# Optimization experiments

Hardware: AMD Instinct MI355X
Metric: run time of the kernel (lower is better)

## Reference

```python
import jax, jax.numpy as jnp
import numpy as np

N, E, F, C, K, H = 100000, 1600000, 64, 32, 8, 36


def setup_inputs() -> dict:
    key = jax.random.key(0)
    ks = jax.random.split(key, 24)
    s = 0.1
    inp = {
        "x": jax.random.normal(ks[0], (N, F), jnp.float32),
        "edge_index": jax.random.randint(ks[1], (2, E), 0, N, dtype=jnp.int32),
        # ChebConv conv1_1: K x [F, H] weights + bias
        "W1_1": jax.random.normal(ks[2], (K, F, H), jnp.float32) * s,
        "b1_1": jnp.zeros((H,), jnp.float32),
        "g1_1": jnp.ones((H,), jnp.float32),
        "be1_1": jnp.zeros((H,), jnp.float32),
        # ChebConv conv1_2: K x [H, H]
        "W1_2": jax.random.normal(ks[3], (K, H, H), jnp.float32) * s,
        "b1_2": jnp.zeros((H,), jnp.float32),
        "g1_2": jnp.ones((H,), jnp.float32),
        "be1_2": jnp.zeros((H,), jnp.float32),
        # GINConv MLP: Linear(F,H) -> ReLU -> Linear(H,H)
        "gin_w1": jax.random.normal(ks[4], (F, H), jnp.float32) * s,
        "gin_b1": jnp.zeros((H,), jnp.float32),
        "gin_w2": jax.random.normal(ks[5], (H, H), jnp.float32) * s,
        "gin_b2": jnp.zeros((H,), jnp.float32),
        "g2": jnp.ones((H,), jnp.float32),
        "be2": jnp.zeros((H,), jnp.float32),
        # conv4: ChebConv K=1 on concat(3H) -> C  (pure linear, no propagation)
        "W4": jax.random.normal(ks[6], (1, 3 * H, C), jnp.float32) * s,
        "b4": jnp.zeros((C,), jnp.float32),
    }
    return inp


def _spmm(w, src, dst, x, n):
    # out[i] = sum_{e: dst_e=i} w_e * x[src_e]
    return jax.ops.segment_sum(w[:, None] * x[src], dst, num_segments=n)


def _cheb(x, src, dst, w, Wk, b):
    # PyG ChebConv with sym norm, lambda_max=2: L_hat = -D^-1/2 A D^-1/2 (loop weight 0)
    n = x.shape[0]
    Kk = Wk.shape[0]
    Tx0 = x
    out = Tx0 @ Wk[0]
    if Kk > 1:
        Tx1 = _spmm(w, src, dst, Tx0, n)
        out = out + Tx1 @ Wk[1]
        for k in range(2, Kk):
            Tx2 = 2.0 * _spmm(w, src, dst, Tx1, n) - Tx0
            out = out + Tx2 @ Wk[k]
            Tx0, Tx1 = Tx1, Tx2
    return out + b


def _bn(x, g, b, eps=1e-5):
    m = jnp.mean(x, axis=0)
    v = jnp.mean(jnp.square(x - m), axis=0)  # biased var, training-mode BN
    return g * (x - m) * jax.lax.rsqrt(v + eps) + b


def reference(x, edge_index, W1_1, b1_1, g1_1, be1_1, W1_2, b1_2, g1_2, be1_2,
              gin_w1, gin_b1, gin_w2, gin_b2, g2, be2, W4, b4):
    src, dst = edge_index[0], edge_index[1]
    n = x.shape[0]
    deg = jax.ops.segment_sum(jnp.ones((src.shape[0],), x.dtype), src, num_segments=n)
    dis = jnp.where(deg > 0, jax.lax.rsqrt(jnp.maximum(deg, 1.0)), 0.0)
    w = -dis[src] * dis[dst]  # scaled Laplacian edge weights

    x1_1 = jax.nn.relu(_bn(_cheb(x, src, dst, w, W1_1, b1_1), g1_1, be1_1))
    x1_2 = jax.nn.relu(_bn(_cheb(x1_1, src, dst, w, W1_2, b1_2), g1_2, be1_2))

    # GINConv (eps=0): nn(x + sum_{j in N(i)} x_j)
    agg = jax.ops.segment_sum(x[src], dst, num_segments=n)
    h = x + agg
    gin = jax.nn.relu(h @ gin_w1 + gin_b1) @ gin_w2 + gin_b2
    x2 = _bn(jax.nn.relu(gin), g2, be2)

    x4 = jnp.concatenate((x1_1, x1_2, x2), axis=1)
    return x4 @ W4[0] + b4
```

## Files before the change

### kernel.cpp

```cpp
#include <hip/hip_runtime.h>

constexpr int N_NODES = 100000;
constexpr int N_EDGES = 1600000;
constexpr int NBK  = 391;
constexpr int NBLK = 640;
constexpr int CHUNK = 2500;
constexpr int LCNT = NBK * NBLK;
constexpr int SCAN_BLKS = (LCNT + 255) / 256;


__device__ __forceinline__ unsigned bf16pack(float a, float b) {
    unsigned ua = __float_as_uint(a), ub = __float_as_uint(b);
    ua += 0x7fffu + ((ua >> 16) & 1u);
    ub += 0x7fffu + ((ub >> 16) & 1u);
    return (ua >> 16) | (ub & 0xffff0000u);
}
__device__ __forceinline__ float bflo(unsigned p) { return __uint_as_float(p << 16); }
__device__ __forceinline__ float bfhi(unsigned p) { return __uint_as_float(p & 0xffff0000u); }

__device__ __forceinline__ int esrc(unsigned v) { return (int)(v & 0x1FFFFu); }
__device__ __forceinline__ float ew(unsigned v) {
    return __uint_as_float(0x80000000u | ((v >> 17) << 16));
}


__global__ __launch_bounds__(256) void part_count_kernel(
    const int* __restrict__ ei, int* __restrict__ cntD, int* __restrict__ cntS) {
    __shared__ int hd[NBK], hs[NBK];
    int tid = threadIdx.x;
    for (int i = tid; i < NBK; i += 256) { hd[i] = 0; hs[i] = 0; }
    __syncthreads();
    int e0 = blockIdx.x * CHUNK;
    for (int e = e0 + tid; e < e0 + CHUNK; e += 256) {
        int s = ei[e], d = ei[N_EDGES + e];
        atomicAdd(&hs[s >> 8], 1);
        atomicAdd(&hd[d >> 8], 1);
    }
    __syncthreads();
    for (int i = tid; i < NBK; i += 256) {
        cntD[i * NBLK + blockIdx.x] = hd[i];
        cntS[i * NBLK + blockIdx.x] = hs[i];
    }
}

__global__ __launch_bounds__(256) void scanA_kernel(const int* __restrict__ in,
                                                    int* __restrict__ out,
                                                    int* __restrict__ bsum, int L) {
    __shared__ int sm[256];
    int i = blockIdx.x * 256 + threadIdx.x;
    int v = (i < L) ? in[i] : 0;
    sm[threadIdx.x] = v;
    __syncthreads();
    for (int off = 1; off < 256; off <<= 1) {
        int t = (threadIdx.x >= off) ? sm[threadIdx.x - off] : 0;
        __syncthreads();
        sm[threadIdx.x] += t;
        __syncthreads();
    }
    if (i < L) out[i] = sm[threadIdx.x] - v;
    if (threadIdx.x == 255) bsum[blockIdx.x] = sm[255];
}

__global__ __launch_bounds__(1024) void scanB_kernel(int* __restrict__ bsum, int nb) {
    __shared__ int sm[1024];
    int t = threadIdx.x;
    int v = (t < nb) ? bsum[t] : 0;
    sm[t] = v;
    __syncthreads();
    for (int off = 1; off < 1024; off <<= 1) {
        int u = (t >= off) ? sm[t - off] : 0;
        __syncthreads();
        sm[t] += u;
        __syncthreads();
    }
    if (t < nb) bsum[t] = sm[t] - v;
}

__global__ __launch_bounds__(256) void scanC_kernel(int* __restrict__ out,
                                                    const int* __restrict__ bsum, int L) {
    int i = blockIdx.x * 256 + threadIdx.x;
    if (i < L) out[i] += bsum[blockIdx.x];
}

__global__ __launch_bounds__(256) void part_scatter_kernel(
    const int* __restrict__ ei, const int* __restrict__ scanD,
    const int* __restrict__ scanS, int2* __restrict__ edgepart,
    int* __restrict__ srcpart) {
    __shared__ int curD[NBK], curS[NBK];
    int tid = threadIdx.x;
    for (int i = tid; i < NBK; i += 256) {
        curD[i] = scanD[i * NBLK + blockIdx.x];
        curS[i] = scanS[i * NBLK + blockIdx.x];
    }
    __syncthreads();
    int e0 = blockIdx.x * CHUNK;
    for (int e = e0 + tid; e < e0 + CHUNK; e += 256) {
        int s = ei[e], d = ei[N_EDGES + e];
        int pd = atomicAdd(&curD[d >> 8], 1);
        edgepart[pd] = make_int2(s, d);
        int ps = atomicAdd(&curS[s >> 8], 1);
        srcpart[ps] = s;
    }
}

__global__ __launch_bounds__(256) void deg_kernel(const int* __restrict__ srcpart,
                                                  const int* __restrict__ scanS,
                                                  float* __restrict__ dis) {
    __shared__ int cnt[256];
    int b = blockIdx.x, tid = threadIdx.x;
    cnt[tid] = 0;
    __syncthreads();
    int beg = scanS[b * NBLK];
    int end = (b + 1 < NBK) ? scanS[(b + 1) * NBLK] : N_EDGES;
    for (int j = beg + tid; j < end; j += 256)
        atomicAdd(&cnt[srcpart[j] & 255], 1);
    __syncthreads();
    int node = b * 256 + tid;
    if (node < N_NODES) dis[node] = cnt[tid] > 0 ? rsqrtf((float)cnt[tid]) : 0.f;
}

__global__ __launch_bounds__(256) void csr_kernel(const int2* __restrict__ edgepart,
                                                  const int* __restrict__ scanD,
                                                  const float* __restrict__ dis,
                                                  int* __restrict__ rp,
                                                  unsigned* __restrict__ csrc) {
    __shared__ int cnt[256];
    __shared__ int lofs[256];
    __shared__ float disl[256];
    int b = blockIdx.x, tid = threadIdx.x;
    int beg = scanD[b * NBLK];
    int end = (b + 1 < NBK) ? scanD[(b + 1) * NBLK] : N_EDGES;
    int node = b * 256 + tid;
    cnt[tid] = 0;
    disl[tid] = (node < N_NODES) ? dis[node] : 0.f;
    __syncthreads();
    for (int j = beg + tid; j < end; j += 256)
        atomicAdd(&cnt[edgepart[j].y & 255], 1);
    __syncthreads();
    int v = cnt[tid];
    lofs[tid] = v;
    __syncthreads();
    for (int off = 1; off < 256; off <<= 1) {
        int t = (tid >= off) ? lofs[tid - off] : 0;
        __syncthreads();
        lofs[tid] += t;
        __syncthreads();
    }
    int myexc = lofs[tid] - v;
    if (node < N_NODES) rp[node] = beg + myexc;
    if (b == NBK - 1 && tid == 0) rp[N_NODES] = N_EDGES;
    __syncthreads();
    lofs[tid] = myexc;
    cnt[tid] = 0;
    __syncthreads();
    for (int j = beg + tid; j < end; j += 256) {
        int2 e = edgepart[j];
        int dl = e.y & 255;
        int pos = beg + lofs[dl] + atomicAdd(&cnt[dl], 1);
        unsigned u = __float_as_uint(-(dis[e.x] * disl[dl]));
        u += 0x7fffu + ((u >> 16) & 1u);
        unsigned wb = (u >> 16) & 0x7FFFu;
        csrc[pos] = (unsigned)e.x | (wb << 17);
    }
}

__global__ void pack_x_kernel(const float* __restrict__ x, uint2* __restrict__ xbf) {
    int i = blockIdx.x * blockDim.x + threadIdx.x;
    if (i >= N_NODES * 16) return;
    float4 v = ((const float4*)x)[i];
    xbf[i] = make_uint2(bf16pack(v.x, v.y), bf16pack(v.z, v.w));
}


template <int FI, int SCALE, bool HAS_B2, bool BN_A, bool FUSE_STATS>
__global__ __launch_bounds__(256) void cheb_step_kernel(
    const int* __restrict__ rp, const unsigned* __restrict__ csrc,
    const uint2* __restrict__ INb, const uint2* __restrict__ B2b,
    const uint2* __restrict__ Ab, const float* __restrict__ W,
    const float* __restrict__ ss, unsigned long long* __restrict__ OUT,
    float* __restrict__ partials) {
    constexpr int RU2 = FI / 4;
    __shared__ float Wl[FI * 36];
    __shared__ float Atile[28][FI + 1];
    __shared__ float ls[72];
    int tid = threadIdx.x;
    for (int i = tid; i < FI * 36; i += 252) Wl[i] = W[i];
    int r0 = blockIdx.x * 28;
    const long long* ab8 = (const long long*)Ab;
    for (int i = tid; i < 28 * RU2; i += 252) {
        int r = i / RU2, u = i % RU2;
        int row = r0 + r;
        long long av = (row < N_NODES) ? ab8[(size_t)row * RU2 + u] : 0LL;
        unsigned lo = (unsigned)av, hi = (unsigned)(av >> 32);
        float f0 = bflo(lo), f1 = bfhi(lo), f2 = bflo(hi), f3 = bfhi(hi);
        if (BN_A) {
            int f = u * 4;
            f0 = fmaxf(fmaf(ss[f + 0], f0, ss[36 + f + 0]), 0.f);
            f1 = fmaxf(fmaf(ss[f + 1], f1, ss[36 + f + 1]), 0.f);
            f2 = fmaxf(fmaf(ss[f + 2], f2, ss[36 + f + 2]), 0.f);
            f3 = fmaxf(fmaf(ss[f + 3], f3, ss[36 + f + 3]), 0.f);
        }
        Atile[r][u * 4 + 0] = f0; Atile[r][u * 4 + 1] = f1;
        Atile[r][u * 4 + 2] = f2; Atile[r][u * 4 + 3] = f3;
    }
    if (FUSE_STATS && tid < 72) ls[tid] = 0.f;
    __syncthreads();
    int r = tid / 9, c = tid % 9;
    int row = r0 + r;
    bool valid = row < N_NODES;
    float ax = 0, ay = 0, az = 0, aw = 0;
    float bx = 0, by = 0, bz = 0, bw = 0;
    float cx = 0, cy = 0, cz = 0, cw = 0;
    float dx = 0, dy = 0, dz = 0, dw = 0;
    if (SCALE != 0 && valid) {
        int beg = rp[row], end = rp[row + 1];
        int j = beg;
        for (; j + 7 < end; j += 8) {
            unsigned v0 = csrc[j],     v1 = csrc[j + 1], v2 = csrc[j + 2], v3 = csrc[j + 3];
            unsigned v4 = csrc[j + 4], v5 = csrc[j + 5], v6 = csrc[j + 6], v7 = csrc[j + 7];
            uint2 u0 = INb[(size_t)esrc(v0) * 9 + c];
            uint2 u1 = INb[(size_t)esrc(v1) * 9 + c];
            uint2 u2 = INb[(size_t)esrc(v2) * 9 + c];
            uint2 u3 = INb[(size_t)esrc(v3) * 9 + c];
            uint2 u4 = INb[(size_t)esrc(v4) * 9 + c];
            uint2 u5 = INb[(size_t)esrc(v5) * 9 + c];
            uint2 u6 = INb[(size_t)esrc(v6) * 9 + c];
            uint2 u7 = INb[(size_t)esrc(v7) * 9 + c];
            float w0 = ew(v0), w1 = ew(v1), w2 = ew(v2), w3 = ew(v3);
            float w4 = ew(v4), w5 = ew(v5), w6 = ew(v6), w7 = ew(v7);
            ax = fmaf(w0, bflo(u0.x), ax); ay = fmaf(w0, bfhi(u0.x), ay);
            az = fmaf(w0, bflo(u0.y), az); aw = fmaf(w0, bfhi(u0.y), aw);
            bx = fmaf(w1, bflo(u1.x), bx); by = fmaf(w1, bfhi(u1.x), by);
            bz = fmaf(w1, bflo(u1.y), bz); bw = fmaf(w1, bfhi(u1.y), bw);
            cx = fmaf(w2, bflo(u2.x), cx); cy = fmaf(w2, bfhi(u2.x), cy);
            cz = fmaf(w2, bflo(u2.y), cz); cw = fmaf(w2, bfhi(u2.y), cw);
            dx = fmaf(w3, bflo(u3.x), dx); dy = fmaf(w3, bfhi(u3.x), dy);
            dz = fmaf(w3, bflo(u3.y), dz); dw = fmaf(w3, bfhi(u3.y), dw);
            ax = fmaf(w4, bflo(u4.x), ax); ay = fmaf(w4, bfhi(u4.x), ay);
            az = fmaf(w4, bflo(u4.y), az); aw = fmaf(w4, bfhi(u4.y), aw);
            bx = fmaf(w5, bflo(u5.x), bx); by = fmaf(w5, bfhi(u5.x), by);
            bz = fmaf(w5, bflo(u5.y), bz); bw = fmaf(w5, bfhi(u5.y), bw);
            cx = fmaf(w6, bflo(u6.x), cx); cy = fmaf(w6, bfhi(u6.x), cy);
            cz = fmaf(w6, bflo(u6.y), cz); cw = fmaf(w6, bfhi(u6.y), cw);
            dx = fmaf(w7, bflo(u7.x), dx); dy = fmaf(w7, bfhi(u7.x), dy);
            dz = fmaf(w7, bflo(u7.y), dz); dw = fmaf(w7, bfhi(u7.y), dw);
        }
        for (; j < end; ++j) {
            unsigned v = csrc[j];
            uint2 u = INb[(size_t)esrc(v) * 9 + c];
            float w = ew(v);
            ax = fmaf(w, bflo(u.x), ax); ay = fmaf(w, bfhi(u.x), ay);
            az = fmaf(w, bflo(u.y), az); aw = fmaf(w, bfhi(u.y), aw);
        }
        ax += bx + cx + dx; ay += by + cy + dy;
        az += bz + cz + dz; aw += bw + cw + dw;
    }
    float px = 0, py = 0, pz = 0, pw = 0;
    const float4* Wl4 = (const float4*)Wl;
#pragma unroll 4
    for (int f = 0; f < FI; ++f) {
        float a = Atile[r][f];
        float4 wv = Wl4[f * 9 + c];
        px = fmaf(a, wv.x, px); py = fmaf(a, wv.y, py);
        pz = fmaf(a, wv.z, pz); pw = fmaf(a, wv.w, pw);
    }
    const float S = (float)SCALE;
    float4 o;
    o.x = fmaf(S, ax, px); o.y = fmaf(S, ay, py);
    o.z = fmaf(S, az, pz); o.w = fmaf(S, aw, pw);
    if (valid) {
        if (HAS_B2) {
            uint2 u = B2b[(size_t)row * 9 + c];
            o.x -= bflo(u.x); o.y -= bfhi(u.x);
            o.z -= bflo(u.y); o.w -= bfhi(u.y);
        }
        unsigned long long pv = (unsigned long long)bf16pack(o.x, o.y)
                              | ((unsigned long long)bf16pack(o.z, o.w) << 32);
        OUT[(size_t)row * 9 + c] = pv;
        if (FUSE_STATS) {
            atomicAdd(&ls[c * 4 + 0], o.x); atomicAdd(&ls[36 + c * 4 + 0], o.x * o.x);
            atomicAdd(&ls[c * 4 + 1], o.y); atomicAdd(&ls[36 + c * 4 + 1], o.y * o.y);
            atomicAdd(&ls[c * 4 + 2], o.z); atomicAdd(&ls[36 + c * 4 + 2], o.z * o.z);
            atomicAdd(&ls[c * 4 + 3], o.w); atomicAdd(&ls[36 + c * 4 + 3], o.w * o.w);
        }
    }
    if (FUSE_STATS) {
        __syncthreads();
        if (tid < 72) partials[blockIdx.x * 72 + tid] = ls[tid];
    }
}


__global__ __launch_bounds__(256) void gin_gather_kernel(
    const int* __restrict__ rp, const unsigned* __restrict__ csrc,
    const uint2* __restrict__ Yb, const float* __restrict__ b1,
    const float* __restrict__ w2, const float* __restrict__ b2,
    unsigned long long* __restrict__ OUT, float* __restrict__ partials) {
    __shared__ float W2l[36 * 36];
    __shared__ float B1l[36], B2l[36];
    __shared__ float M1t[28][37];
    __shared__ float ls[72];
    int tid = threadIdx.x;
    for (int i = tid; i < 36 * 36; i += 252) W2l[i] = w2[i];
    if (tid < 36) { B1l[tid] = b1[tid]; B2l[tid] = b2[tid]; }
    if (tid < 72) ls[tid] = 0.f;
    __syncthreads();
    int r = tid / 9, c = tid % 9;
    int row = blockIdx.x * 28 + r;
    bool valid = row < N_NODES;
    float ax = 0, ay = 0, az = 0, aw = 0;
    float bx = 0, by = 0, bz = 0, bw = 0;
    float cx = 0, cy = 0, cz = 0, cw = 0;
    float dx = 0, dy = 0, dz = 0, dw = 0;
    if (valid) {
        uint2 us = Yb[(size_t)row * 9 + c];
        ax = bflo(us.x); ay = bfhi(us.x); az = bflo(us.y); aw = bfhi(us.y);
        int beg = rp[row], end = rp[row + 1];
        int j = beg;
        for (; j + 7 < end; j += 8) {
            int s0 = esrc(csrc[j]),     s1 = esrc(csrc[j + 1]);
            int s2 = esrc(csrc[j + 2]), s3 = esrc(csrc[j + 3]);
            int s4 = esrc(csrc[j + 4]), s5 = esrc(csrc[j + 5]);
            int s6 = esrc(csrc[j + 6]), s7 = esrc(csrc[j + 7]);
            uint2 u0 = Yb[(size_t)s0 * 9 + c];
            uint2 u1 = Yb[(size_t)s1 * 9 + c];
            uint2 u2 = Yb[(size_t)s2 * 9 + c];
            uint2 u3 = Yb[(size_t)s3 * 9 + c];
            uint2 u4 = Yb[(size_t)s4 * 9 + c];
            uint2 u5 = Yb[(size_t)s5 * 9 + c];
            uint2 u6 = Yb[(size_t)s6 * 9 + c];
            uint2 u7 = Yb[(size_t)s7 * 9 + c];
            ax += bflo(u0.x) + bflo(u4.x); ay += bfhi(u0.x) + bfhi(u4.x);
            az += bflo(u0.y) + bflo(u4.y); aw += bfhi(u0.y) + bfhi(u4.y);
            bx += bflo(u1.x) + bflo(u5.x); by += bfhi(u1.x) + bfhi(u5.x);
            bz += bflo(u1.y) + bflo(u5.y); bw += bfhi(u1.y) + bfhi(u5.y);
            cx += bflo(u2.x) + bflo(u6.x); cy += bfhi(u2.x) + bfhi(u6.x);
            cz += bflo(u2.y) + bflo(u6.y); cw += bfhi(u2.y) + bfhi(u6.y);
            dx += bflo(u3.x) + bflo(u7.x); dy += bfhi(u3.x) + bfhi(u7.x);
            dz += bflo(u3.y) + bflo(u7.y); dw += bfhi(u3.y) + bfhi(u7.y);
        }
        for (; j < end; ++j) {
            uint2 u = Yb[(size_t)esrc(csrc[j]) * 9 + c];
            ax += bflo(u.x); ay += bfhi(u.x);
            az += bflo(u.y); aw += bfhi(u.y);
        }
        ax += bx + cx + dx; ay += by + cy + dy;
        az += bz + cz + dz; aw += bw + cw + dw;
    }
    float m0 = fmaxf(ax + B1l[c * 4 + 0], 0.f);
    float m1 = fmaxf(ay + B1l[c * 4 + 1], 0.f);
    float m2 = fmaxf(az + B1l[c * 4 + 2], 0.f);
    float m3 = fmaxf(aw + B1l[c * 4 + 3], 0.f);
    M1t[r][c * 4 + 0] = m0; M1t[r][c * 4 + 1] = m1;
    M1t[r][c * 4 + 2] = m2; M1t[r][c * 4 + 3] = m3;
    __syncthreads();
    float o0 = B2l[c * 4 + 0], o1 = B2l[c * 4 + 1];
    float o2 = B2l[c * 4 + 2], o3 = B2l[c * 4 + 3];
    const float4* W2l4 = (const float4*)W2l;
#pragma unroll 4
    for (int f = 0; f < 36; ++f) {
        float a = M1t[r][f];
        float4 wv = W2l4[f * 9 + c];
        o0 = fmaf(a, wv.x, o0); o1 = fmaf(a, wv.y, o1);
        o2 = fmaf(a, wv.z, o2); o3 = fmaf(a, wv.w, o3);
    }
    o0 = fmaxf(o0, 0.f); o1 = fmaxf(o1, 0.f);
    o2 = fmaxf(o2, 0.f); o3 = fmaxf(o3, 0.f);
    if (valid) {
        unsigned long long pv = (unsigned long long)bf16pack(o0, o1)
                              | ((unsigned long long)bf16pack(o2, o3) << 32);
        OUT[(size_t)row * 9 + c] = pv;
        atomicAdd(&ls[c * 4 + 0], o0); atomicAdd(&ls[36 + c * 4 + 0], o0 * o0);
        atomicAdd(&ls[c * 4 + 1], o1); atomicAdd(&ls[36 + c * 4 + 1], o1 * o1);
        atomicAdd(&ls[c * 4 + 2], o2); atomicAdd(&ls[36 + c * 4 + 2], o2 * o2);
        atomicAdd(&ls[c * 4 + 3], o3); atomicAdd(&ls[36 + c * 4 + 3], o3 * o3);
    }
    __syncthreads();
    if (tid < 72) partials[blockIdx.x * 72 + tid] = ls[tid];
}


__global__ __launch_bounds__(256) void finalize_kernel(
    const float* __restrict__ partials, int nb, const float* __restrict__ g,
    const float* __restrict__ be, float* __restrict__ ss) {
    __shared__ float rs[256], rq[256];
    int c = blockIdx.x;
    int t = threadIdx.x;
    float s = 0.f, q = 0.f;
    for (int i = t; i < nb; i += 256) {
        s += partials[i * 72 + c];
        q += partials[i * 72 + c + 36];
    }
    rs[t] = s; rq[t] = q;
    __syncthreads();
    for (int off = 128; off > 0; off >>= 1) {
        if (t < off) { rs[t] += rs[t + off]; rq[t] += rq[t + off]; }
        __syncthreads();
    }
    if (t == 0) {
        float m = rs[0] / (float)N_NODES;
        float v = rq[0] / (float)N_NODES - m * m;
        float sc = g[c] * rsqrtf(v + 1e-5f);
        ss[c] = sc;
        ss[36 + c] = be[c] - m * sc;
    }
}


__global__ __launch_bounds__(256) void fused3_kernel(
    const uint2* __restrict__ X1b, const float* __restrict__ ssA,
    const uint2* __restrict__ X2b, const float* __restrict__ ssB,
    const uint2* __restrict__ X3b, const float* __restrict__ ssC,
    const float* __restrict__ W, const float* __restrict__ b,
    float* __restrict__ out) {
    __shared__ float Wl[108 * 32];
    __shared__ float Al[32][109];
    int tid = threadIdx.x;
    for (int i = tid; i < 108 * 32; i += 256) Wl[i] = W[i];
    int r0 = blockIdx.x * 32;
    for (int i = tid; i < 32 * 108; i += 256) {
        int r = i / 108, f = i % 108;
        int row = r0 + r;
        float v = 0.f;
        if (row < N_NODES) {
            int t = f / 36, ff = f % 36;
            const unsigned short* base =
                (const unsigned short*)(t == 0 ? X1b : (t == 1 ? X2b : X3b));
            float xv = __uint_as_float((unsigned)base[(size_t)row * 36 + ff] << 16);
            if (t == 0)      v = fmaxf(fmaf(ssA[ff], xv, ssA[36 + ff]), 0.f);
            else if (t == 1) v = fmaxf(fmaf(ssB[ff], xv, ssB[36 + ff]), 0.f);
            else             v = fmaf(ssC[ff], xv, ssC[36 + ff]);
        }
        Al[r][f] = v;
    }
    __syncthreads();
    int r = tid >> 3, q = tid & 7;
    int row = r0 + r;
    if (row >= N_NODES) return;
    float acc[4];
#pragma unroll
    for (int j = 0; j < 4; ++j) acc[j] = b[q * 4 + j];
    for (int f = 0; f < 108; ++f) {
        float a = Al[r][f];
#pragma unroll
        for (int j = 0; j < 4; ++j)
            acc[j] = fmaf(a, Wl[f * 32 + q * 4 + j], acc[j]);
    }
#pragma unroll
    for (int j = 0; j < 4; ++j) out[(size_t)row * 32 + q * 4 + j] = acc[j];
}


extern "C" void kernel_launch(void* const* d_in, const int* in_sizes, int n_in,
                              void* d_out, int out_size, void* d_ws, size_t ws_size,
                              hipStream_t stream) {
    const float* x      = (const float*)d_in[0];
    const int*   ei     = (const int*)d_in[1];
    const float* W1_1   = (const float*)d_in[2];
    const float* g1_1   = (const float*)d_in[4];
    const float* be1_1  = (const float*)d_in[5];
    const float* W1_2   = (const float*)d_in[6];
    const float* g1_2   = (const float*)d_in[8];
    const float* be1_2  = (const float*)d_in[9];
    const float* gin_w1 = (const float*)d_in[10];
    const float* gin_b1 = (const float*)d_in[11];
    const float* gin_w2 = (const float*)d_in[12];
    const float* gin_b2 = (const float*)d_in[13];
    const float* g2     = (const float*)d_in[14];
    const float* be2    = (const float*)d_in[15];
    const float* W4     = (const float*)d_in[16];
    const float* b4     = (const float*)d_in[17];
    float* out = (float*)d_out;

    char* ws = (char*)d_ws;
    size_t off = 0;
    auto alloc = [&](size_t bytes) -> char* {
        char* p = ws + off;
        off = (off + bytes + 255) & ~(size_t)255;
        return p;
    };
    int*   cntD  = (int*)alloc((size_t)LCNT * 4);
    int*   cntS  = (int*)alloc((size_t)LCNT * 4);
    int*   bsum  = (int*)alloc(1024 * 4);
    int*   rp    = (int*)alloc((size_t)(N_NODES + 1) * 4);
    float* dis   = (float*)alloc((size_t)N_NODES * 4);
    int2*  edgepart = (int2*)alloc((size_t)N_EDGES * 8);
    int*   srcpart  = (int*)alloc((size_t)N_EDGES * 4);
    unsigned* csrc = (unsigned*)alloc((size_t)N_EDGES * 4);
    float* ssA   = (float*)alloc(72 * 4);
    float* ssB   = (float*)alloc(72 * 4);
    float* ssC   = (float*)alloc(72 * 4);
    float* partials = (float*)alloc((size_t)6250 * 72 * 4);
    constexpr size_t NBBF = (size_t)N_NODES * 72;
    uint2* xbf = (uint2*)alloc((size_t)N_NODES * 128);
    uint2* R0  = (uint2*)alloc(NBBF);
    uint2* R1  = (uint2*)alloc(NBBF);
    uint2* R2  = (uint2*)alloc(NBBF);
    uint2* X1b = (uint2*)alloc(NBBF);
    uint2* X2b = (uint2*)alloc(NBBF);
    uint2* X3b = (uint2*)alloc(NBBF);
    if (off > ws_size) return;

    part_count_kernel<<<NBLK, 256, 0, stream>>>(ei, cntD, cntS);
    scanA_kernel<<<SCAN_BLKS, 256, 0, stream>>>(cntD, cntD, bsum, LCNT);
    scanB_kernel<<<1, 1024, 0, stream>>>(bsum, SCAN_BLKS);
    scanC_kernel<<<SCAN_BLKS, 256, 0, stream>>>(cntD, bsum, LCNT);
    scanA_kernel<<<SCAN_BLKS, 256, 0, stream>>>(cntS, cntS, bsum, LCNT);
    scanB_kernel<<<1, 1024, 0, stream>>>(bsum, SCAN_BLKS);
    scanC_kernel<<<SCAN_BLKS, 256, 0, stream>>>(cntS, bsum, LCNT);
    part_scatter_kernel<<<NBLK, 256, 0, stream>>>(ei, cntD, cntS, edgepart, srcpart);
    deg_kernel<<<NBK, 256, 0, stream>>>(srcpart, cntS, dis);
    csr_kernel<<<NBK, 256, 0, stream>>>(edgepart, cntD, dis, rp, csrc);
    pack_x_kernel<<<(N_NODES * 16 + 255) / 256, 256, 0, stream>>>(x, xbf);

    const int STEP_BLKS = (N_NODES + 27) / 28;
    const int F3_BLKS   = (N_NODES + 31) / 32;

    auto U64 = [](uint2* p) { return (unsigned long long*)p; };

    cheb_step_kernel<64, 0, false, false, false><<<STEP_BLKS, 252, 0, stream>>>(
        rp, csrc, nullptr, nullptr, xbf, W1_1 + 7 * 2304, nullptr, U64(R0), nullptr);
    cheb_step_kernel<64, 2, false, false, false><<<STEP_BLKS, 252, 0, stream>>>(
        rp, csrc, R0, nullptr, xbf, W1_1 + 6 * 2304, nullptr, U64(R1), nullptr);
    cheb_step_kernel<64, 2, true, false, false><<<STEP_BLKS, 252, 0, stream>>>(
        rp, csrc, R1, R0, xbf, W1_1 + 5 * 2304, nullptr, U64(R2), nullptr);
    cheb_step_kernel<64, 2, true, false, false><<<STEP_BLKS, 252, 0, stream>>>(
        rp, csrc, R2, R1, xbf, W1_1 + 4 * 2304, nullptr, U64(R0), nullptr);
    cheb_step_kernel<64, 2, true, false, false><<<STEP_BLKS, 252, 0, stream>>>(
        rp, csrc, R0, R2, xbf, W1_1 + 3 * 2304, nullptr, U64(R1), nullptr);
    cheb_step_kernel<64, 2, true, false, false><<<STEP_BLKS, 252, 0, stream>>>(
        rp, csrc, R1, R0, xbf, W1_1 + 2 * 2304, nullptr, U64(R2), nullptr);
    cheb_step_kernel<64, 2, true, false, false><<<STEP_BLKS, 252, 0, stream>>>(
        rp, csrc, R2, R1, xbf, W1_1 + 1 * 2304, nullptr, U64(R0), nullptr);
    cheb_step_kernel<64, 1, true, false, true><<<STEP_BLKS, 252, 0, stream>>>(
        rp, csrc, R0, R2, xbf, W1_1 + 0 * 2304, nullptr, U64(X1b), partials);
    finalize_kernel<<<36, 256, 0, stream>>>(partials, STEP_BLKS, g1_1, be1_1, ssA);

    cheb_step_kernel<36, 0, false, true, false><<<STEP_BLKS, 252, 0, stream>>>(
        rp, csrc, nullptr, nullptr, X1b, W1_2 + 7 * 1296, ssA, U64(R0), nullptr);
    cheb_step_kernel<36, 2, false, true, false><<<STEP_BLKS, 252, 0, stream>>>(
        rp, csrc, R0, nullptr, X1b, W1_2 + 6 * 1296, ssA, U64(R1), nullptr);
    cheb_step_kernel<36, 2, true, true, false><<<STEP_BLKS, 252, 0, stream>>>(
        rp, csrc, R1, R0, X1b, W1_2 + 5 * 1296, ssA, U64(R2), nullptr);
    cheb_step_kernel<36, 2, true, true, false><<<STEP_BLKS, 252, 0, stream>>>(
        rp, csrc, R2, R1, X1b, W1_2 + 4 * 1296, ssA, U64(R0), nullptr);
    cheb_step_kernel<36, 2, true, true, false><<<STEP_BLKS, 252, 0, stream>>>(
        rp, csrc, R0, R2, X1b, W1_2 + 3 * 1296, ssA, U64(R1), nullptr);
    cheb_step_kernel<36, 2, true, true, false><<<STEP_BLKS, 252, 0, stream>>>(
        rp, csrc, R1, R0, X1b, W1_2 + 2 * 1296, ssA, U64(R2), nullptr);
    cheb_step_kernel<36, 2, true, true, false><<<STEP_BLKS, 252, 0, stream>>>(
        rp, csrc, R2, R1, X1b, W1_2 + 1 * 1296, ssA, U64(R0), nullptr);
    cheb_step_kernel<36, 1, true, true, true><<<STEP_BLKS, 252, 0, stream>>>(
        rp, csrc, R0, R2, X1b, W1_2 + 0 * 1296, ssA, U64(X2b), partials);
    finalize_kernel<<<36, 256, 0, stream>>>(partials, STEP_BLKS, g1_2, be1_2, ssB);

    cheb_step_kernel<64, 0, false, false, false><<<STEP_BLKS, 252, 0, stream>>>(
        rp, csrc, nullptr, nullptr, xbf, gin_w1, nullptr, U64(R0), nullptr);
    gin_gather_kernel<<<STEP_BLKS, 252, 0, stream>>>(rp, csrc, R0, gin_b1,
                                                     gin_w2, gin_b2, U64(X3b), partials);
    finalize_kernel<<<36, 256, 0, stream>>>(partials, STEP_BLKS, g2, be2, ssC);

    fused3_kernel<<<F3_BLKS, 256, 0, stream>>>(X1b, ssA, X2b, ssB, X3b, ssC, W4, b4, out);
}
```

Baseline: 920.0 us.

## Split hidden features into three 12-wide slices to shrink gather working set

Intermediate Chebyshev buffers move from a row-major 36-feature bf16 layout to three slice-major planes of 12 features. Each propagation kernel runs once per slice, so each gathered slice buffer (about 2.4MB) fits in cache better during the random neighbour gathers. The GIN path is also split into a slice-wise gather and a separate slice-wise second linear with bias, ReLU and stats. The cost is three times as many launches, and every slice recomputes the dense A·W projection and rereads the CSR structure.

```diff
diff --git a/kernel.cpp b/kernel.cpp
--- a/kernel.cpp
+++ b/kernel.cpp
@@ -7,6 +7,7 @@
 constexpr int CHUNK = 2500;
 constexpr int LCNT = NBK * NBLK;
 constexpr int SCAN_BLKS = (LCNT + 255) / 256;
+constexpr size_t NS3 = (size_t)N_NODES * 3;
 
 
 __device__ __forceinline__ unsigned bf16pack(float a, float b) {
@@ -172,25 +173,31 @@
 }
 
 
-template <int FI, int SCALE, bool HAS_B2, bool BN_A, bool FUSE_STATS>
-__global__ __launch_bounds__(256) void cheb_step_kernel(
+template <int FI, int SCALE, bool HAS_B2, bool BN_A, bool BIAS_RELU, bool FUSE_STATS>
+__global__ __launch_bounds__(256) void cstep_kernel(
     const int* __restrict__ rp, const unsigned* __restrict__ csrc,
-    const uint2* __restrict__ INb, const uint2* __restrict__ B2b,
+    const uint2* __restrict__ INs, const uint2* __restrict__ B2s,
     const uint2* __restrict__ Ab, const float* __restrict__ W,
-    const float* __restrict__ ss, unsigned long long* __restrict__ OUT,
-    float* __restrict__ partials) {
+    const float* __restrict__ ss, const float* __restrict__ bias,
+    unsigned long long* __restrict__ OUTs, float* __restrict__ partials, int s) {
     constexpr int RU2 = FI / 4;
-    __shared__ float Wl[FI * 36];
-    __shared__ float Atile[28][FI + 1];
-    __shared__ float ls[72];
+    __shared__ float Wl[FI * 12];
+    __shared__ float Atile[84][FI + 1];
+    __shared__ float ls[24];
     int tid = threadIdx.x;
-    for (int i = tid; i < FI * 36; i += 252) Wl[i] = W[i];
-    int r0 = blockIdx.x * 28;
+    for (int i = tid; i < FI * 12; i += 252)
+        Wl[i] = W[(i / 12) * 36 + s * 12 + (i % 12)];
+    int r0 = blockIdx.x * 84;
     const long long* ab8 = (const long long*)Ab;
-    for (int i = tid; i < 28 * RU2; i += 252) {
+    for (int i = tid; i < 84 * RU2; i += 252) {
         int r = i / RU2, u = i % RU2;
         int row = r0 + r;
-        long long av = (row < N_NODES) ? ab8[(size_t)row * RU2 + u] : 0LL;
+        long long av = 0;
+        if (row < N_NODES) {
+            size_t idx = (FI == 64) ? ((size_t)row * 16 + u)
+                                    : ((size_t)(u / 3) * NS3 + (size_t)row * 3 + (u % 3));
+            av = ab8[idx];
+        }
         unsigned lo = (unsigned)av, hi = (unsigned)(av >> 32);
         float f0 = bflo(lo), f1 = bfhi(lo), f2 = bflo(hi), f3 = bfhi(hi);
         if (BN_A) {
@@ -203,9 +210,9 @@
         Atile[r][u * 4 + 0] = f0; Atile[r][u * 4 + 1] = f1;
         Atile[r][u * 4 + 2] = f2; Atile[r][u * 4 + 3] = f3;
     }
-    if (FUSE_STATS && tid < 72) ls[tid] = 0.f;
-    __syncthreads();
-    int r = tid / 9, c = tid % 9;
+    if (FUSE_STATS && tid < 24) ls[tid] = 0.f;
+    __syncthreads();
+    int r = tid / 3, c = tid % 3;
     int row = r0 + r;
     bool valid = row < N_NODES;
     float ax = 0, ay = 0, az = 0, aw = 0;
@@ -218,14 +225,14 @@
         for (; j + 7 < end; j += 8) {
             unsigned v0 = csrc[j],     v1 = csrc[j + 1], v2 = csrc[j + 2], v3 = csrc[j + 3];
             unsigned v4 = csrc[j + 4], v5 = csrc[j + 5], v6 = csrc[j + 6], v7 = csrc[j + 7];
-            uint2 u0 = INb[(size_t)esrc(v0) * 9 + c];
-            uint2 u1 = INb[(size_t)esrc(v1) * 9 + c];
-            uint2 u2 = INb[(size_t)esrc(v2) * 9 + c];
-            uint2 u3 = INb[(size_t)esrc(v3) * 9 + c];
-            uint2 u4 = INb[(size_t)esrc(v4) * 9 + c];
-            uint2 u5 = INb[(size_t)esrc(v5) * 9 + c];
-            uint2 u6 = INb[(size_t)esrc(v6) * 9 + c];
-            uint2 u7 = INb[(size_t)esrc(v7) * 9 + c];
+            uint2 u0 = INs[(size_t)esrc(v0) * 3 + c];
+            uint2 u1 = INs[(size_t)esrc(v1) * 3 + c];
+            uint2 u2 = INs[(size_t)esrc(v2) * 3 + c];
+            uint2 u3 = INs[(size_t)esrc(v3) * 3 + c];
+            uint2 u4 = INs[(size_t)esrc(v4) * 3 + c];
+            uint2 u5 = INs[(size_t)esrc(v5) * 3 + c];
+            uint2 u6 = INs[(size_t)esrc(v6) * 3 + c];
+            uint2 u7 = INs[(size_t)esrc(v7) * 3 + c];
             float w0 = ew(v0), w1 = ew(v1), w2 = ew(v2), w3 = ew(v3);
             float w4 = ew(v4), w5 = ew(v5), w6 = ew(v6), w7 = ew(v7);
             ax = fmaf(w0, bflo(u0.x), ax); ay = fmaf(w0, bfhi(u0.x), ay);
@@ -247,7 +254,7 @@
         }
         for (; j < end; ++j) {
             unsigned v = csrc[j];
-            uint2 u = INb[(size_t)esrc(v) * 9 + c];
+            uint2 u = INs[(size_t)esrc(v) * 3 + c];
             float w = ew(v);
             ax = fmaf(w, bflo(u.x), ax); ay = fmaf(w, bfhi(u.x), ay);
             az = fmaf(w, bflo(u.y), az); aw = fmaf(w, bfhi(u.y), aw);
@@ -260,123 +267,94 @@
 #pragma unroll 4
     for (int f = 0; f < FI; ++f) {
         float a = Atile[r][f];
-        float4 wv = Wl4[f * 9 + c];
+        float4 wv = Wl4[f * 3 + c];
         px = fmaf(a, wv.x, px); py = fmaf(a, wv.y, py);
         pz = fmaf(a, wv.z, pz); pw = fmaf(a, wv.w, pw);
     }
     const float S = (float)SCALE;
-    float4 o;
-    o.x = fmaf(S, ax, px); o.y = fmaf(S, ay, py);
-    o.z = fmaf(S, az, pz); o.w = fmaf(S, aw, pw);
+    float ox = fmaf(S, ax, px), oy = fmaf(S, ay, py);
+    float oz = fmaf(S, az, pz), ow = fmaf(S, aw, pw);
     if (valid) {
         if (HAS_B2) {
-            uint2 u = B2b[(size_t)row * 9 + c];
-            o.x -= bflo(u.x); o.y -= bfhi(u.x);
-            o.z -= bflo(u.y); o.w -= bfhi(u.y);
-        }
-        unsigned long long pv = (unsigned long long)bf16pack(o.x, o.y)
-                              | ((unsigned long long)bf16pack(o.z, o.w) << 32);
-        OUT[(size_t)row * 9 + c] = pv;
+            uint2 u = B2s[(size_t)row * 3 + c];
+            ox -= bflo(u.x); oy -= bfhi(u.x);
+            oz -= bflo(u.y); ow -= bfhi(u.y);
+        }
+        if (BIAS_RELU) {
+            int cb = s * 12 + c * 4;
+            ox = fmaxf(ox + bias[cb + 0], 0.f); oy = fmaxf(oy + bias[cb + 1], 0.f);
+            oz = fmaxf(oz + bias[cb + 2], 0.f); ow = fmaxf(ow + bias[cb + 3], 0.f);
+        }
+        unsigned long long pv = (unsigned long long)bf16pack(ox, oy)
+                              | ((unsigned long long)bf16pack(oz, ow) << 32);
+        OUTs[(size_t)row * 3 + c] = pv;
         if (FUSE_STATS) {
-            atomicAdd(&ls[c * 4 + 0], o.x); atomicAdd(&ls[36 + c * 4 + 0], o.x * o.x);
-            atomicAdd(&ls[c * 4 + 1], o.y); atomicAdd(&ls[36 + c * 4 + 1], o.y * o.y);
-            atomicAdd(&ls[c * 4 + 2], o.z); atomicAdd(&ls[36 + c * 4 + 2], o.z * o.z);
-            atomicAdd(&ls[c * 4 + 3], o.w); atomicAdd(&ls[36 + c * 4 + 3], o.w * o.w);
+            atomicAdd(&ls[c * 4 + 0], ox); atomicAdd(&ls[12 + c * 4 + 0], ox * ox);
+            atomicAdd(&ls[c * 4 + 1], oy); atomicAdd(&ls[12 + c * 4 + 1], oy * oy);
+            atomicAdd(&ls[c * 4 + 2], oz); atomicAdd(&ls[12 + c * 4 + 2], oz * oz);
+            atomicAdd(&ls[c * 4 + 3], ow); atomicAdd(&ls[12 + c * 4 + 3], ow * ow);
         }
     }
     if (FUSE_STATS) {
         __syncthreads();
-        if (tid < 72) partials[blockIdx.x * 72 + tid] = ls[tid];
-    }
-}
-
-
-__global__ __launch_bounds__(256) void gin_gather_kernel(
+        if (tid < 12) {
+            partials[(size_t)blockIdx.x * 72 + s * 12 + tid] = ls[tid];
+            partials[(size_t)blockIdx.x * 72 + 36 + s * 12 + tid] = ls[12 + tid];
+        }
+    }
+}
+
+
+__global__ __launch_bounds__(256) void ginstep_kernel(
     const int* __restrict__ rp, const unsigned* __restrict__ csrc,
-    const uint2* __restrict__ Yb, const float* __restrict__ b1,
-    const float* __restrict__ w2, const float* __restrict__ b2,
-    unsigned long long* __restrict__ OUT, float* __restrict__ partials) {
-    __shared__ float W2l[36 * 36];
-    __shared__ float B1l[36], B2l[36];
-    __shared__ float M1t[28][37];
-    __shared__ float ls[72];
+    const uint2* __restrict__ Ys, const float* __restrict__ b1,
+    unsigned long long* __restrict__ OUTs, int s) {
     int tid = threadIdx.x;
-    for (int i = tid; i < 36 * 36; i += 252) W2l[i] = w2[i];
-    if (tid < 36) { B1l[tid] = b1[tid]; B2l[tid] = b2[tid]; }
-    if (tid < 72) ls[tid] = 0.f;
-    __syncthreads();
-    int r = tid / 9, c = tid % 9;
-    int row = blockIdx.x * 28 + r;
-    bool valid = row < N_NODES;
-    float ax = 0, ay = 0, az = 0, aw = 0;
+    int r = tid / 3, c = tid % 3;
+    int row = blockIdx.x * 84 + r;
+    if (row >= N_NODES) return;
+    uint2 us = Ys[(size_t)row * 3 + c];
+    float ax = bflo(us.x), ay = bfhi(us.x), az = bflo(us.y), aw = bfhi(us.y);
     float bx = 0, by = 0, bz = 0, bw = 0;
     float cx = 0, cy = 0, cz = 0, cw = 0;
     float dx = 0, dy = 0, dz = 0, dw = 0;
-    if (valid) {
-        uint2 us = Yb[(size_t)row * 9 + c];
-        ax = bflo(us.x); ay = bfhi(us.x); az = bflo(us.y); aw = bfhi(us.y);
-        int beg = rp[row], end = rp[row + 1];
-        int j = beg;
-        for (; j + 7 < end; j += 8) {
-            int s0 = esrc(csrc[j]),     s1 = esrc(csrc[j + 1]);
-            int s2 = esrc(csrc[j + 2]), s3 = esrc(csrc[j + 3]);
-            int s4 = esrc(csrc[j + 4]), s5 = esrc(csrc[j + 5]);
-            int s6 = esrc(csrc[j + 6]), s7 = esrc(csrc[j + 7]);
-            uint2 u0 = Yb[(size_t)s0 * 9 + c];
-            uint2 u1 = Yb[(size_t)s1 * 9 + c];
-            uint2 u2 = Yb[(size_t)s2 * 9 + c];
-            uint2 u3 = Yb[(size_t)s3 * 9 + c];
-            uint2 u4 = Yb[(size_t)s4 * 9 + c];
-            uint2 u5 = Yb[(size_t)s5 * 9 + c];
-            uint2 u6 = Yb[(size_t)s6 * 9 + c];
-            uint2 u7 = Yb[(size_t)s7 * 9 + c];
-            ax += bflo(u0.x) + bflo(u4.x); ay += bfhi(u0.x) + bfhi(u4.x);
-            az += bflo(u0.y) + bflo(u4.y); aw += bfhi(u0.y) + bfhi(u4.y);
-            bx += bflo(u1.x) + bflo(u5.x); by += bfhi(u1.x) + bfhi(u5.x);
-            bz += bflo(u1.y) + bflo(u5.y); bw += bfhi(u1.y) + bfhi(u5.y);
-            cx += bflo(u2.x) + bflo(u6.x); cy += bfhi(u2.x) + bfhi(u6.x);
-            cz += bflo(u2.y) + bflo(u6.y); cw += bfhi(u2.y) + bfhi(u6.y);
-            dx += bflo(u3.x) + bflo(u7.x); dy += bfhi(u3.x) + bfhi(u7.x);
-            dz += bflo(u3.y) + bflo(u7.y); dw += bfhi(u3.y) + bfhi(u7.y);
-        }
-        for (; j < end; ++j) {
-            uint2 u = Yb[(size_t)esrc(csrc[j]) * 9 + c];
-            ax += bflo(u.x); ay += bfhi(u.x);
-            az += bflo(u.y); aw += bfhi(u.y);
-        }
-        ax += bx + cx + dx; ay += by + cy + dy;
-        az += bz + cz + dz; aw += bw + cw + dw;
-    }
-    float m0 = fmaxf(ax + B1l[c * 4 + 0], 0.f);
-    float m1 = fmaxf(ay + B1l[c * 4 + 1], 0.f);
-    float m2 = fmaxf(az + B1l[c * 4 + 2], 0.f);
-    float m3 = fmaxf(aw + B1l[c * 4 + 3], 0.f);
-    M1t[r][c * 4 + 0] = m0; M1t[r][c * 4 + 1] = m1;
-    M1t[r][c * 4 + 2] = m2; M1t[r][c * 4 + 3] = m3;
-    __syncthreads();
-    float o0 = B2l[c * 4 + 0], o1 = B2l[c * 4 + 1];
-    float o2 = B2l[c * 4 + 2], o3 = B2l[c * 4 + 3];
-    const float4* W2l4 = (const float4*)W2l;
-#pragma unroll 4
-    for (int f = 0; f < 36; ++f) {
-        float a = M1t[r][f];
-        float4 wv = W2l4[f * 9 + c];
-        o0 = fmaf(a, wv.x, o0); o1 = fmaf(a, wv.y, o1);
-        o2 = fmaf(a, wv.z, o2); o3 = fmaf(a, wv.w, o3);
-    }
-    o0 = fmaxf(o0, 0.f); o1 = fmaxf(o1, 0.f);
-    o2 = fmaxf(o2, 0.f); o3 = fmaxf(o3, 0.f);
-    if (valid) {
-        unsigned long long pv = (unsigned long long)bf16pack(o0, o1)
-                              | ((unsigned long long)bf16pack(o2, o3) << 32);
-        OUT[(size_t)row * 9 + c] = pv;
-        atomicAdd(&ls[c * 4 + 0], o0); atomicAdd(&ls[36 + c * 4 + 0], o0 * o0);
-        atomicAdd(&ls[c * 4 + 1], o1); atomicAdd(&ls[36 + c * 4 + 1], o1 * o1);
-        atomicAdd(&ls[c * 4 + 2], o2); atomicAdd(&ls[36 + c * 4 + 2], o2 * o2);
-        atomicAdd(&ls[c * 4 + 3], o3); atomicAdd(&ls[36 + c * 4 + 3], o3 * o3);
-    }
-    __syncthreads();
-    if (tid < 72) partials[blockIdx.x * 72 + tid] = ls[tid];
+    int beg = rp[row], end = rp[row + 1];
+    int j = beg;
+    for (; j + 7 < end; j += 8) {
+        int s0 = esrc(csrc[j]),     s1 = esrc(csrc[j + 1]);
+        int s2 = esrc(csrc[j + 2]), s3 = esrc(csrc[j + 3]);
+        int s4 = esrc(csrc[j + 4]), s5 = esrc(csrc[j + 5]);
+        int s6 = esrc(csrc[j + 6]), s7 = esrc(csrc[j + 7]);
+        uint2 u0 = Ys[(size_t)s0 * 3 + c];
+        uint2 u1 = Ys[(size_t)s1 * 3 + c];
+        uint2 u2 = Ys[(size_t)s2 * 3 + c];
+        uint2 u3 = Ys[(size_t)s3 * 3 + c];
+        uint2 u4 = Ys[(size_t)s4 * 3 + c];
+        uint2 u5 = Ys[(size_t)s5 * 3 + c];
+        uint2 u6 = Ys[(size_t)s6 * 3 + c];
+        uint2 u7 = Ys[(size_t)s7 * 3 + c];
+        ax += bflo(u0.x) + bflo(u4.x); ay += bfhi(u0.x) + bfhi(u4.x);
+        az += bflo(u0.y) + bflo(u4.y); aw += bfhi(u0.y) + bfhi(u4.y);
+        bx += bflo(u1.x) + bflo(u5.x); by += bfhi(u1.x) + bfhi(u5.x);
+        bz += bflo(u1.y) + bflo(u5.y); bw += bfhi(u1.y) + bfhi(u5.y);
+        cx += bflo(u2.x) + bflo(u6.x); cy += bfhi(u2.x) + bfhi(u6.x);
+        cz += bflo(u2.y) + bflo(u6.y); cw += bfhi(u2.y) + bfhi(u6.y);
+        dx += bflo(u3.x) + bflo(u7.x); dy += bfhi(u3.x) + bfhi(u7.x);
+        dz += bflo(u3.y) + bflo(u7.y); dw += bfhi(u3.y) + bfhi(u7.y);
+    }
+    for (; j < end; ++j) {
+        uint2 u = Ys[(size_t)esrc(csrc[j]) * 3 + c];
+        ax += bflo(u.x); ay += bfhi(u.x);
+        az += bflo(u.y); aw += bfhi(u.y);
+    }
+    ax += bx + cx + dx; ay += by + cy + dy;
+    az += bz + cz + dz; aw += bw + cw + dw;
+    int cb = s * 12 + c * 4;
+    ax = fmaxf(ax + b1[cb + 0], 0.f); ay = fmaxf(ay + b1[cb + 1], 0.f);
+    az = fmaxf(az + b1[cb + 2], 0.f); aw = fmaxf(aw + b1[cb + 3], 0.f);
+    unsigned long long pv = (unsigned long long)bf16pack(ax, ay)
+                          | ((unsigned long long)bf16pack(az, aw) << 32);
+    OUTs[(size_t)row * 3 + c] = pv;
 }
 
 
@@ -388,8 +366,8 @@
     int t = threadIdx.x;
     float s = 0.f, q = 0.f;
     for (int i = t; i < nb; i += 256) {
-        s += partials[i * 72 + c];
-        q += partials[i * 72 + c + 36];
+        s += partials[(size_t)i * 72 + c];
+        q += partials[(size_t)i * 72 + c + 36];
     }
     rs[t] = s; rq[t] = q;
     __syncthreads();
@@ -423,10 +401,10 @@
         int row = r0 + r;
         float v = 0.f;
         if (row < N_NODES) {
-            int t = f / 36, ff = f % 36;
-            const unsigned short* base =
-                (const unsigned short*)(t == 0 ? X1b : (t == 1 ? X2b : X3b));
-            float xv = __uint_as_float((unsigned)base[(size_t)row * 36 + ff] << 16);
+            int t = f / 36, ff = f % 36, sl = ff / 12, w = ff % 12;
+            const uint2* base = (t == 0 ? X1b : (t == 1 ? X2b : X3b)) + (size_t)sl * NS3;
+            unsigned short u16 = ((const unsigned short*)base)[(size_t)row * 12 + w];
+            float xv = __uint_as_float((unsigned)u16 << 16);
             if (t == 0)      v = fmaxf(fmaf(ssA[ff], xv, ssA[36 + ff]), 0.f);
             else if (t == 1) v = fmaxf(fmaf(ssB[ff], xv, ssB[36 + ff]), 0.f);
             else             v = fmaf(ssC[ff], xv, ssC[36 + ff]);
@@ -490,8 +468,8 @@
     float* ssA   = (float*)alloc(72 * 4);
     float* ssB   = (float*)alloc(72 * 4);
     float* ssC   = (float*)alloc(72 * 4);
-    float* partials = (float*)alloc((size_t)6250 * 72 * 4);
-    constexpr size_t NBBF = (size_t)N_NODES * 72;
+    float* partials = (float*)alloc((size_t)4096 * 72 * 4);
+    constexpr size_t NBBF = NS3 * 3 * 8;
     uint2* xbf = (uint2*)alloc((size_t)N_NODES * 128);
     uint2* R0  = (uint2*)alloc(NBBF);
     uint2* R1  = (uint2*)alloc(NBBF);
@@ -513,52 +491,61 @@
     csr_kernel<<<NBK, 256, 0, stream>>>(edgepart, cntD, dis, rp, csrc);
     pack_x_kernel<<<(N_NODES * 16 + 255) / 256, 256, 0, stream>>>(x, xbf);
 
-    const int STEP_BLKS = (N_NODES + 27) / 28;
-    const int F3_BLKS   = (N_NODES + 31) / 32;
-
-    auto U64 = [](uint2* p) { return (unsigned long long*)p; };
-
-    cheb_step_kernel<64, 0, false, false, false><<<STEP_BLKS, 252, 0, stream>>>(
-        rp, csrc, nullptr, nullptr, xbf, W1_1 + 7 * 2304, nullptr, U64(R0), nullptr);
-    cheb_step_kernel<64, 2, false, false, false><<<STEP_BLKS, 252, 0, stream>>>(
-        rp, csrc, R0, nullptr, xbf, W1_1 + 6 * 2304, nullptr, U64(R1), nullptr);
-    cheb_step_kernel<64, 2, true, false, false><<<STEP_BLKS, 252, 0, stream>>>(
-        rp, csrc, R1, R0, xbf, W1_1 + 5 * 2304, nullptr, U64(R2), nullptr);
-    cheb_step_kernel<64, 2, true, false, false><<<STEP_BLKS, 252, 0, stream>>>(
-        rp, csrc, R2, R1, xbf, W1_1 + 4 * 2304, nullptr, U64(R0), nullptr);
-    cheb_step_kernel<64, 2, true, false, false><<<STEP_BLKS, 252, 0, stream>>>(
-        rp, csrc, R0, R2, xbf, W1_1 + 3 * 2304, nullptr, U64(R1), nullptr);
-    cheb_step_kernel<64, 2, true, false, false><<<STEP_BLKS, 252, 0, stream>>>(
-        rp, csrc, R1, R0, xbf, W1_1 + 2 * 2304, nullptr, U64(R2), nullptr);
-    cheb_step_kernel<64, 2, true, false, false><<<STEP_BLKS, 252, 0, stream>>>(
-        rp, csrc, R2, R1, xbf, W1_1 + 1 * 2304, nullptr, U64(R0), nullptr);
-    cheb_step_kernel<64, 1, true, false, true><<<STEP_BLKS, 252, 0, stream>>>(
-        rp, csrc, R0, R2, xbf, W1_1 + 0 * 2304, nullptr, U64(X1b), partials);
-    finalize_kernel<<<36, 256, 0, stream>>>(partials, STEP_BLKS, g1_1, be1_1, ssA);
-
-    cheb_step_kernel<36, 0, false, true, false><<<STEP_BLKS, 252, 0, stream>>>(
-        rp, csrc, nullptr, nullptr, X1b, W1_2 + 7 * 1296, ssA, U64(R0), nullptr);
-    cheb_step_kernel<36, 2, false, true, false><<<STEP_BLKS, 252, 0, stream>>>(
-        rp, csrc, R0, nullptr, X1b, W1_2 + 6 * 1296, ssA, U64(R1), nullptr);
-    cheb_step_kernel<36, 2, true, true, false><<<STEP_BLKS, 252, 0, stream>>>(
-        rp, csrc, R1, R0, X1b, W1_2 + 5 * 1296, ssA, U64(R2), nullptr);
-    cheb_step_kernel<36, 2, true, true, false><<<STEP_BLKS, 252, 0, stream>>>(
-        rp, csrc, R2, R1, X1b, W1_2 + 4 * 1296, ssA, U64(R0), nullptr);
-    cheb_step_kernel<36, 2, true, true, false><<<STEP_BLKS, 252, 0, stream>>>(
-        rp, csrc, R0, R2, X1b, W1_2 + 3 * 1296, ssA, U64(R1), nullptr);
-    cheb_step_kernel<36, 2, true, true, false><<<STEP_BLKS, 252, 0, stream>>>(
-        rp, csrc, R1, R0, X1b, W1_2 + 2 * 1296, ssA, U64(R2), nullptr);
-    cheb_step_kernel<36, 2, true, true, false><<<STEP_BLKS, 252, 0, stream>>>(
-        rp, csrc, R2, R1, X1b, W1_2 + 1 * 1296, ssA, U64(R0), nullptr);
-    cheb_step_kernel<36, 1, true, true, true><<<STEP_BLKS, 252, 0, stream>>>(
-        rp, csrc, R0, R2, X1b, W1_2 + 0 * 1296, ssA, U64(X2b), partials);
-    finalize_kernel<<<36, 256, 0, stream>>>(partials, STEP_BLKS, g1_2, be1_2, ssB);
-
-    cheb_step_kernel<64, 0, false, false, false><<<STEP_BLKS, 252, 0, stream>>>(
-        rp, csrc, nullptr, nullptr, xbf, gin_w1, nullptr, U64(R0), nullptr);
-    gin_gather_kernel<<<STEP_BLKS, 252, 0, stream>>>(rp, csrc, R0, gin_b1,
-                                                     gin_w2, gin_b2, U64(X3b), partials);
-    finalize_kernel<<<36, 256, 0, stream>>>(partials, STEP_BLKS, g2, be2, ssC);
+    const int GBLKS = (N_NODES + 83) / 84;
+    const int F3_BLKS = (N_NODES + 31) / 32;
+
+    auto SL  = [&](uint2* p, int s) { return (const uint2*)(p + (size_t)s * NS3); };
+    auto SLO = [&](uint2* p, int s) { return (unsigned long long*)(p + (size_t)s * NS3); };
+
+    for (int s = 0; s < 3; ++s) {
+        cstep_kernel<64, 0, false, false, false, false><<<GBLKS, 252, 0, stream>>>(
+            rp, csrc, nullptr, nullptr, xbf, W1_1 + 7 * 2304, nullptr, nullptr, SLO(R0, s), nullptr, s);
+        cstep_kernel<64, 2, false, false, false, false><<<GBLKS, 252, 0, stream>>>(
+            rp, csrc, SL(R0, s), nullptr, xbf, W1_1 + 6 * 2304, nullptr, nullptr, SLO(R1, s), nullptr, s);
+        cstep_kernel<64, 2, true, false, false, false><<<GBLKS, 252, 0, stream>>>(
+            rp, csrc, SL(R1, s), SL(R0, s), xbf, W1_1 + 5 * 2304, nullptr, nullptr, SLO(R2, s), nullptr, s);
+        cstep_kernel<64, 2, true, false, false, false><<<GBLKS, 252, 0, stream>>>(
+            rp, csrc, SL(R2, s), SL(R1, s), xbf, W1_1 + 4 * 2304, nullptr, nullptr, SLO(R0, s), nullptr, s);
+        cstep_kernel<64, 2, true, false, false, false><<<GBLKS, 252, 0, stream>>>(
+            rp, csrc, SL(R0, s), SL(R2, s), xbf, W1_1 + 3 * 2304, nullptr, nullptr, SLO(R1, s), nullptr, s);
+        cstep_kernel<64, 2, true, false, false, false><<<GBLKS, 252, 0, stream>>>(
+            rp, csrc, SL(R1, s), SL(R0, s), xbf, W1_1 + 2 * 2304, nullptr, nullptr, SLO(R2, s), nullptr, s);
+        cstep_kernel<64, 2, true, false, false, false><<<GBLKS, 252, 0, stream>>>(
+            rp, csrc, SL(R2, s), SL(R1, s), xbf, W1_1 + 1 * 2304, nullptr, nullptr, SLO(R0, s), nullptr, s);
+        cstep_kernel<64, 1, true, false, false, true><<<GBLKS, 252, 0, stream>>>(
+            rp, csrc, SL(R0, s), SL(R2, s), xbf, W1_1 + 0 * 2304, nullptr, nullptr, SLO(X1b, s), partials, s);
+    }
+    finalize_kernel<<<36, 256, 0, stream>>>(partials, GBLKS, g1_1, be1_1, ssA);
+
+    for (int s = 0; s < 3; ++s) {
+        cstep_kernel<36, 0, false, true, false, false><<<GBLKS, 252, 0, stream>>>(
+            rp, csrc, nullptr, nullptr, X1b, W1_2 + 7 * 1296, ssA, nullptr, SLO(R0, s), nullptr, s);
+        cstep_kernel<36, 2, false, true, false, false><<<GBLKS, 252, 0, stream>>>(
+            rp, csrc, SL(R0, s), nullptr, X1b, W1_2 + 6 * 1296, ssA, nullptr, SLO(R1, s), nullptr, s);
+        cstep_kernel<36, 2, true, true, false, false><<<GBLKS, 252, 0, stream>>>(
+            rp, csrc, SL(R1, s), SL(R0, s), X1b, W1_2 + 5 * 1296, ssA, nullptr, SLO(R2, s), nullptr, s);
+        cstep_kernel<36, 2, true, true, false, false><<<GBLKS, 252, 0, stream>>>(
+            rp, csrc, SL(R2, s), SL(R1, s), X1b, W1_2 + 4 * 1296, ssA, nullptr, SLO(R0, s), nullptr, s);
+        cstep_kernel<36, 2, true, true, false, false><<<GBLKS, 252, 0, stream>>>(
+            rp, csrc, SL(R0, s), SL(R2, s), X1b, W1_2 + 3 * 1296, ssA, nullptr, SLO(R1, s), nullptr, s);
+        cstep_kernel<36, 2, true, true, false, false><<<GBLKS, 252, 0, stream>>>(
+            rp, csrc, SL(R1, s), SL(R0, s), X1b, W1_2 + 2 * 1296, ssA, nullptr, SLO(R2, s), nullptr, s);
+        cstep_kernel<36, 2, true, true, false, false><<<GBLKS, 252, 0, stream>>>(
+            rp, csrc, SL(R2, s), SL(R1, s), X1b, W1_2 + 1 * 1296, ssA, nullptr, SLO(R0, s), nullptr, s);
+        cstep_kernel<36, 1, true, true, false, true><<<GBLKS, 252, 0, stream>>>(
+            rp, csrc, SL(R0, s), SL(R2, s), X1b, W1_2 + 0 * 1296, ssA, nullptr, SLO(X2b, s), partials, s);
+    }
+    finalize_kernel<<<36, 256, 0, stream>>>(partials, GBLKS, g1_2, be1_2, ssB);
+
+    for (int s = 0; s < 3; ++s)
+        cstep_kernel<64, 0, false, false, false, false><<<GBLKS, 252, 0, stream>>>(
+            rp, csrc, nullptr, nullptr, xbf, gin_w1, nullptr, nullptr, SLO(R0, s), nullptr, s);
+    for (int s = 0; s < 3; ++s)
+        ginstep_kernel<<<GBLKS, 252, 0, stream>>>(rp, csrc, SL(R0, s), gin_b1, SLO(R1, s), s);
+    for (int s = 0; s < 3; ++s)
+        cstep_kernel<36, 0, false, false, true, true><<<GBLKS, 252, 0, stream>>>(
+            rp, csrc, nullptr, nullptr, R1, gin_w2, nullptr, gin_b2, SLO(X3b, s), partials, s);
+    finalize_kernel<<<36, 256, 0, stream>>>(partials, GBLKS, g2, be2, ssC);
 
     fused3_kernel<<<F3_BLKS, 256, 0, stream>>>(X1b, ssA, X2b, ssB, X3b, ssC, W4, b4, out);
 }
```

After: 1.191 ms. 29.5% more time.
